# Performance work log

Hardware: AMD Instinct MI355X
Metric: run time of the kernel (lower is better)

The kernel has to match this reference:

```python
import jax, jax.numpy as jnp
import numpy as np

MODEL_SR = 50000
START_FRAME = int(MODEL_SR * 0.25)   # 12500
END_FRAME = int(MODEL_SR * 2.75)     # 137500
N_TAPS = 10000
BATCH = 64
T = 150000


def setup_inputs() -> dict:
    key = jax.random.key(0)
    k1, k2 = jax.random.split(key)
    x = jax.random.normal(k1, (BATCH, T), dtype=jnp.float32)          # mono audio clips
    ir = jax.random.normal(k2, (N_TAPS, 2), dtype=jnp.float32)        # BRIR: (taps, L/R)
    return {"x": x, "ir": ir}


def reference(x, ir):
    # Faithful to torch: ir flipped along taps, then cross-correlated by conv1d
    # (lax.conv_general_dilated is also cross-correlation), i.e. true convolution.
    n_taps = ir.shape[0]
    w = jnp.flip(ir, axis=0).T[:, None, :]              # (C_out=2, C_in=1, K)
    xp = jnp.pad(x, ((0, 0), (n_taps - 1, 0)))[:, None, :]  # left-pad K-1 -> (N, 1, T+K-1)
    y = jax.lax.conv_general_dilated(
        xp, w,
        window_strides=(1,),
        padding="VALID",
        dimension_numbers=("NCW", "OIW", "NCW"),
    )                                                    # (N, 2, T)
    return y[:, :, START_FRAME:END_FRAME]                # (N, 2, 125000)
```

## Files before the change

kernel.cpp:

```cpp
#include <hip/hip_runtime.h>


#define K_TAPS  10000
#define T_LEN   150000
#define OUT_T0  12500
#define OUT_T1  137500
#define OUT_LEN 125000
#define BATCH   64

#define TM    256
#define KC    32
#define NC    321
#define D0    10016
#define RROWS 288
#define ACOLS 40
#define XCOLS 40

typedef short  bf16x8 __attribute__((ext_vector_type(8)));
typedef float  f32x4  __attribute__((ext_vector_type(4)));

__device__ __forceinline__ unsigned f2bf(float f) {
    unsigned u = __builtin_bit_cast(unsigned, f);
    return (u + 0x7FFFu + ((u >> 16) & 1u)) >> 16;
}

__global__ __launch_bounds__(512, 4) void spatialize_mfma(
    const float* __restrict__ x, const float* __restrict__ ir,
    float* __restrict__ out)
{
    __shared__ ushort a_lds[2][RROWS][ACOLS];
    __shared__ ushort xb[2][BATCH][XCOLS];

    const int tid  = threadIdx.x;
    const int lane = tid & 63;
    const int wid  = tid >> 6;
    const int wm   = wid >> 1;
    const int wn   = wid & 1;
    const int t0   = OUT_T0 + blockIdx.x * TM;
    const int p_start = t0 - D0;

    const int bch = tid >> 8;
    const int bm  = (tid >> 3) & 31;
    const int bk0 = (tid & 7) * 4;

    const int sb = tid >> 3;
    const int sg = tid & 7;

#pragma unroll
    for (int s = 0; s < TM / KC; ++s) {
        const int m  = s * KC + bm;
        const int pr = KC + m;
        const int db = D0 + m - bk0;
        unsigned h0 = (db-0 >= 0 && db-0 < K_TAPS) ? f2bf(ir[2*(db-0)+bch]) : 0u;
        unsigned h1 = (db-1 >= 0 && db-1 < K_TAPS) ? f2bf(ir[2*(db-1)+bch]) : 0u;
        unsigned h2 = (db-2 >= 0 && db-2 < K_TAPS) ? f2bf(ir[2*(db-2)+bch]) : 0u;
        unsigned h3 = (db-3 >= 0 && db-3 < K_TAPS) ? f2bf(ir[2*(db-3)+bch]) : 0u;
        uint2 w; w.x = h0 | (h1 << 16); w.y = h2 | (h3 << 16);
        *reinterpret_cast<uint2*>(&a_lds[bch][pr][bk0]) = w;
    }
    {
        const float4 v = *reinterpret_cast<const float4*>(
            &x[(size_t)sb * T_LEN + p_start + sg * 4]);
        uint2 w; w.x = f2bf(v.x) | (f2bf(v.y) << 16);
                 w.y = f2bf(v.z) | (f2bf(v.w) << 16);
        *reinterpret_cast<uint2*>(&xb[0][sb][sg * 4]) = w;
    }
    __syncthreads();

    f32x4 acc[4][2][2];
#pragma unroll
    for (int mt = 0; mt < 4; ++mt)
#pragma unroll
        for (int nt = 0; nt < 2; ++nt)
#pragma unroll
            for (int ch = 0; ch < 2; ++ch)
                acc[mt][nt][ch] = (f32x4){0.f, 0.f, 0.f, 0.f};

    int vbase = KC;

    const int koff = 8 * (lane >> 4);
    const int lrow = lane & 15;

    for (int i = 0; i < NC; ++i) {
        const int  cur  = i & 1;
        const bool more = (i + 1 < NC);
        int vb2 = vbase - KC; if (vb2 < 0) vb2 += RROWS;

        float4 xv = make_float4(0.f, 0.f, 0.f, 0.f);
        float hv0 = 0.f, hv1 = 0.f, hv2 = 0.f, hv3 = 0.f;
        if (more) {
            const int p0n = p_start + (i + 1) * KC;
            xv = *reinterpret_cast<const float4*>(
                &x[(size_t)sb * T_LEN + p0n + sg * 4]);
            const int db = (D0 - (i + 1) * KC) + bm - bk0;
            hv0 = (db-0 >= 0 && db-0 < K_TAPS) ? ir[2*(db-0)+bch] : 0.f;
            hv1 = (db-1 >= 0 && db-1 < K_TAPS) ? ir[2*(db-1)+bch] : 0.f;
            hv2 = (db-2 >= 0 && db-2 < K_TAPS) ? ir[2*(db-2)+bch] : 0.f;
            hv3 = (db-3 >= 0 && db-3 < K_TAPS) ? ir[2*(db-3)+bch] : 0.f;
        }

        bf16x8 bfr0 = *reinterpret_cast<const bf16x8*>(&xb[cur][wn*32 +      lrow][koff]);
        bf16x8 bfr1 = *reinterpret_cast<const bf16x8*>(&xb[cur][wn*32 + 16 + lrow][koff]);
#pragma unroll
        for (int mt = 0; mt < 4; ++mt) {
            int g = vbase + wm * 64 + mt * 16; if (g >= RROWS) g -= RROWS;
            const int row = g + lrow;
#pragma unroll
            for (int ch = 0; ch < 2; ++ch) {
                bf16x8 af = *reinterpret_cast<const bf16x8*>(&a_lds[ch][row][koff]);
                acc[mt][0][ch] = __builtin_amdgcn_mfma_f32_16x16x32_bf16(
                    af, bfr0, acc[mt][0][ch], 0, 0, 0);
                acc[mt][1][ch] = __builtin_amdgcn_mfma_f32_16x16x32_bf16(
                    af, bfr1, acc[mt][1][ch], 0, 0, 0);
            }
        }

        if (more) {
            uint2 wx; wx.x = f2bf(xv.x) | (f2bf(xv.y) << 16);
                      wx.y = f2bf(xv.z) | (f2bf(xv.w) << 16);
            *reinterpret_cast<uint2*>(&xb[cur ^ 1][sb][sg * 4]) = wx;
            uint2 wa; wa.x = f2bf(hv0) | (f2bf(hv1) << 16);
                      wa.y = f2bf(hv2) | (f2bf(hv3) << 16);
            *reinterpret_cast<uint2*>(&a_lds[bch][vb2 + bm][bk0]) = wa;
            vbase = vb2;
        }
        __syncthreads();
    }

    const int r4 = (lane >> 4) * 4;
#pragma unroll
    for (int mt = 0; mt < 4; ++mt) {
        const int t4 = t0 + (wm * 4 + mt) * 16 + r4;
        if (t4 < OUT_T1) {
#pragma unroll
            for (int nt = 0; nt < 2; ++nt) {
                const int b = wn * 32 + nt * 16 + lrow;
#pragma unroll
                for (int ch = 0; ch < 2; ++ch) {
                    float4 v = make_float4(acc[mt][nt][ch][0], acc[mt][nt][ch][1],
                                           acc[mt][nt][ch][2], acc[mt][nt][ch][3]);
                    *reinterpret_cast<float4*>(
                        &out[(size_t)b * (2 * OUT_LEN) + (size_t)ch * OUT_LEN +
                             (t4 - OUT_T0)]) = v;
                }
            }
        }
    }
}

extern "C" void kernel_launch(void* const* d_in, const int* in_sizes, int n_in,
                              void* d_out, int out_size, void* d_ws, size_t ws_size,
                              hipStream_t stream)
{
    (void)in_sizes; (void)n_in; (void)d_ws; (void)ws_size; (void)out_size;
    const float* x  = (const float*)d_in[0];
    const float* ir = (const float*)d_in[1];
    float* out      = (float*)d_out;

    dim3 grid((OUT_LEN + TM - 1) / TM);
    dim3 block(512);
    hipLaunchKernelGGL(spatialize_mfma, grid, block, 0, stream, x, ir, out);
}
```

Before: 491.6 us.

## Precompute bf16 Toeplitz filter table in global memory and widen per-wave tiles

```diff
diff --git a/kernel.cpp b/kernel.cpp
--- a/kernel.cpp
+++ b/kernel.cpp
@@ -10,10 +10,14 @@
 
 #define TM    256
 #define KC    32
+#define D0    10016
 #define NC    321
-#define D0    10016
-#define RROWS 288
-#define ACOLS 40
+#define NMAX  (D0 + TM - 1)
+#define NTAB  10528
+#define CS_BYTES  (NTAB * 2)
+#define CH_STRIDE (8 * CS_BYTES)
+#define TAB_BYTES (2 * CH_STRIDE)
+
 #define XCOLS 40
 
 typedef short  bf16x8 __attribute__((ext_vector_type(8)));
@@ -24,124 +28,127 @@
     return (u + 0x7FFFu + ((u >> 16) & 1u)) >> 16;
 }
 
-__global__ __launch_bounds__(512, 4) void spatialize_mfma(
-    const float* __restrict__ x, const float* __restrict__ ir,
+__global__ __launch_bounds__(256) void build_tab(
+    const float* __restrict__ ir, ushort* __restrict__ tab)
+{
+    const int m = blockIdx.x * 256 + threadIdx.x;
+    if (m >= NTAB) return;
+    const int y   = blockIdx.y;
+    const int ch  = y >> 3;
+    const int rho = y & 7;
+    const int d   = NMAX - m - rho;
+    const float v = (d >= 0 && d < K_TAPS) ? ir[2 * d + ch] : 0.f;
+    tab[(size_t)ch * (8 * NTAB) + (size_t)rho * NTAB + m] = (ushort)f2bf(v);
+}
+
+__global__ __launch_bounds__(256, 2) void spatialize_mfma2(
+    const float* __restrict__ x, const ushort* __restrict__ tab,
     float* __restrict__ out)
 {
-    __shared__ ushort a_lds[2][RROWS][ACOLS];
     __shared__ ushort xb[2][BATCH][XCOLS];
 
     const int tid  = threadIdx.x;
     const int lane = tid & 63;
-    const int wid  = tid >> 6;
-    const int wm   = wid >> 1;
-    const int wn   = wid & 1;
-    const int t0   = OUT_T0 + blockIdx.x * TM;
+    const int wm   = tid >> 6;
+    const int lrow = lane & 15;
+    const int koff = (lane >> 4) * 8;
+
+    const int nwg = gridDim.x;
+    const int q8 = nwg >> 3, r8 = nwg & 7;
+    const int xcd = blockIdx.x & 7, loc = blockIdx.x >> 3;
+    const int tile = (xcd < r8 ? xcd * (q8 + 1) : r8 * (q8 + 1) + (xcd - r8) * q8) + loc;
+
+    const int t0      = OUT_T0 + tile * TM;
     const int p_start = t0 - D0;
 
-    const int bch = tid >> 8;
-    const int bm  = (tid >> 3) & 31;
-    const int bk0 = (tid & 7) * 4;
+    const int s0 = NMAX - D0 - wm * 64 - lrow + koff;
+    int aoff = (s0 & 7) * CS_BYTES + ((s0 >> 3) << 4);
+    const char* tA0 = (const char*)tab;
+    const char* tA1 = (const char*)tab + CH_STRIDE;
 
-    const int sb = tid >> 3;
-    const int sg = tid & 7;
+    const int sb = tid >> 2;
+    const int sg = tid & 3;
+    const float* xrow = x + (size_t)sb * T_LEN + p_start + sg * 8;
 
-#pragma unroll
-    for (int s = 0; s < TM / KC; ++s) {
-        const int m  = s * KC + bm;
-        const int pr = KC + m;
-        const int db = D0 + m - bk0;
-        unsigned h0 = (db-0 >= 0 && db-0 < K_TAPS) ? f2bf(ir[2*(db-0)+bch]) : 0u;
-        unsigned h1 = (db-1 >= 0 && db-1 < K_TAPS) ? f2bf(ir[2*(db-1)+bch]) : 0u;
-        unsigned h2 = (db-2 >= 0 && db-2 < K_TAPS) ? f2bf(ir[2*(db-2)+bch]) : 0u;
-        unsigned h3 = (db-3 >= 0 && db-3 < K_TAPS) ? f2bf(ir[2*(db-3)+bch]) : 0u;
-        uint2 w; w.x = h0 | (h1 << 16); w.y = h2 | (h3 << 16);
-        *reinterpret_cast<uint2*>(&a_lds[bch][pr][bk0]) = w;
-    }
     {
-        const float4 v = *reinterpret_cast<const float4*>(
-            &x[(size_t)sb * T_LEN + p_start + sg * 4]);
-        uint2 w; w.x = f2bf(v.x) | (f2bf(v.y) << 16);
-                 w.y = f2bf(v.z) | (f2bf(v.w) << 16);
-        *reinterpret_cast<uint2*>(&xb[0][sb][sg * 4]) = w;
+        const float4 v0 = *(const float4*)(xrow);
+        const float4 v1 = *(const float4*)(xrow + 4);
+        uint4 w;
+        w.x = f2bf(v0.x) | (f2bf(v0.y) << 16);
+        w.y = f2bf(v0.z) | (f2bf(v0.w) << 16);
+        w.z = f2bf(v1.x) | (f2bf(v1.y) << 16);
+        w.w = f2bf(v1.z) | (f2bf(v1.w) << 16);
+        *(uint4*)&xb[0][sb][sg * 8] = w;
     }
     __syncthreads();
 
-    f32x4 acc[4][2][2];
+    f32x4 acc[4][4][2];
 #pragma unroll
     for (int mt = 0; mt < 4; ++mt)
 #pragma unroll
-        for (int nt = 0; nt < 2; ++nt)
+        for (int nt = 0; nt < 4; ++nt)
 #pragma unroll
             for (int ch = 0; ch < 2; ++ch)
                 acc[mt][nt][ch] = (f32x4){0.f, 0.f, 0.f, 0.f};
 
-    int vbase = KC;
-
-    const int koff = 8 * (lane >> 4);
-    const int lrow = lane & 15;
-
     for (int i = 0; i < NC; ++i) {
         const int  cur  = i & 1;
         const bool more = (i + 1 < NC);
-        int vb2 = vbase - KC; if (vb2 < 0) vb2 += RROWS;
 
-        float4 xv = make_float4(0.f, 0.f, 0.f, 0.f);
-        float hv0 = 0.f, hv1 = 0.f, hv2 = 0.f, hv3 = 0.f;
+        float4 v0, v1;
         if (more) {
-            const int p0n = p_start + (i + 1) * KC;
-            xv = *reinterpret_cast<const float4*>(
-                &x[(size_t)sb * T_LEN + p0n + sg * 4]);
-            const int db = (D0 - (i + 1) * KC) + bm - bk0;
-            hv0 = (db-0 >= 0 && db-0 < K_TAPS) ? ir[2*(db-0)+bch] : 0.f;
-            hv1 = (db-1 >= 0 && db-1 < K_TAPS) ? ir[2*(db-1)+bch] : 0.f;
-            hv2 = (db-2 >= 0 && db-2 < K_TAPS) ? ir[2*(db-2)+bch] : 0.f;
-            hv3 = (db-3 >= 0 && db-3 < K_TAPS) ? ir[2*(db-3)+bch] : 0.f;
+            const float* xp = xrow + (i + 1) * KC;
+            v0 = *(const float4*)(xp);
+            v1 = *(const float4*)(xp + 4);
         }
 
-        bf16x8 bfr0 = *reinterpret_cast<const bf16x8*>(&xb[cur][wn*32 +      lrow][koff]);
-        bf16x8 bfr1 = *reinterpret_cast<const bf16x8*>(&xb[cur][wn*32 + 16 + lrow][koff]);
+        bf16x8 af0[4], af1[4];
 #pragma unroll
         for (int mt = 0; mt < 4; ++mt) {
-            int g = vbase + wm * 64 + mt * 16; if (g >= RROWS) g -= RROWS;
-            const int row = g + lrow;
+            af0[mt] = *(const bf16x8*)(tA0 + (aoff - 32 * mt));
+            af1[mt] = *(const bf16x8*)(tA1 + (aoff - 32 * mt));
+        }
+        bf16x8 bfr[4];
 #pragma unroll
-            for (int ch = 0; ch < 2; ++ch) {
-                bf16x8 af = *reinterpret_cast<const bf16x8*>(&a_lds[ch][row][koff]);
-                acc[mt][0][ch] = __builtin_amdgcn_mfma_f32_16x16x32_bf16(
-                    af, bfr0, acc[mt][0][ch], 0, 0, 0);
-                acc[mt][1][ch] = __builtin_amdgcn_mfma_f32_16x16x32_bf16(
-                    af, bfr1, acc[mt][1][ch], 0, 0, 0);
+        for (int nt = 0; nt < 4; ++nt)
+            bfr[nt] = *(const bf16x8*)&xb[cur][nt * 16 + lrow][koff];
+
+#pragma unroll
+        for (int mt = 0; mt < 4; ++mt)
+#pragma unroll
+            for (int nt = 0; nt < 4; ++nt) {
+                acc[mt][nt][0] = __builtin_amdgcn_mfma_f32_16x16x32_bf16(
+                    af0[mt], bfr[nt], acc[mt][nt][0], 0, 0, 0);
+                acc[mt][nt][1] = __builtin_amdgcn_mfma_f32_16x16x32_bf16(
+                    af1[mt], bfr[nt], acc[mt][nt][1], 0, 0, 0);
             }
-        }
 
         if (more) {
-            uint2 wx; wx.x = f2bf(xv.x) | (f2bf(xv.y) << 16);
-                      wx.y = f2bf(xv.z) | (f2bf(xv.w) << 16);
-            *reinterpret_cast<uint2*>(&xb[cur ^ 1][sb][sg * 4]) = wx;
-            uint2 wa; wa.x = f2bf(hv0) | (f2bf(hv1) << 16);
-                      wa.y = f2bf(hv2) | (f2bf(hv3) << 16);
-            *reinterpret_cast<uint2*>(&a_lds[bch][vb2 + bm][bk0]) = wa;
-            vbase = vb2;
+            uint4 w;
+            w.x = f2bf(v0.x) | (f2bf(v0.y) << 16);
+            w.y = f2bf(v0.z) | (f2bf(v0.w) << 16);
+            w.z = f2bf(v1.x) | (f2bf(v1.y) << 16);
+            w.w = f2bf(v1.z) | (f2bf(v1.w) << 16);
+            *(uint4*)&xb[cur ^ 1][sb][sg * 8] = w;
         }
         __syncthreads();
+        aoff += 64;
     }
 
     const int r4 = (lane >> 4) * 4;
 #pragma unroll
     for (int mt = 0; mt < 4; ++mt) {
-        const int t4 = t0 + (wm * 4 + mt) * 16 + r4;
+        const int t4 = t0 + wm * 64 + mt * 16 + r4;
         if (t4 < OUT_T1) {
 #pragma unroll
-            for (int nt = 0; nt < 2; ++nt) {
-                const int b = wn * 32 + nt * 16 + lrow;
+            for (int nt = 0; nt < 4; ++nt) {
+                const int b = nt * 16 + lrow;
 #pragma unroll
                 for (int ch = 0; ch < 2; ++ch) {
-                    float4 v = make_float4(acc[mt][nt][ch][0], acc[mt][nt][ch][1],
-                                           acc[mt][nt][ch][2], acc[mt][nt][ch][3]);
-                    *reinterpret_cast<float4*>(
-                        &out[(size_t)b * (2 * OUT_LEN) + (size_t)ch * OUT_LEN +
-                             (t4 - OUT_T0)]) = v;
+                    const f32x4 a = acc[mt][nt][ch];
+                    *(float4*)&out[(size_t)b * (2 * OUT_LEN) +
+                                   (size_t)ch * OUT_LEN + (t4 - OUT_T0)] =
+                        make_float4(a[0], a[1], a[2], a[3]);
                 }
             }
         }
@@ -152,12 +159,15 @@
                               void* d_out, int out_size, void* d_ws, size_t ws_size,
                               hipStream_t stream)
 {
-    (void)in_sizes; (void)n_in; (void)d_ws; (void)ws_size; (void)out_size;
+    (void)in_sizes; (void)n_in; (void)out_size; (void)ws_size;
     const float* x  = (const float*)d_in[0];
     const float* ir = (const float*)d_in[1];
     float* out      = (float*)d_out;
+    ushort* tab     = (ushort*)d_ws;
+
+    dim3 gt((NTAB + 255) / 256, 16);
+    hipLaunchKernelGGL(build_tab, gt, dim3(256), 0, stream, ir, tab);
 
     dim3 grid((OUT_LEN + TM - 1) / TM);
-    dim3 block(512);
-    hipLaunchKernelGGL(spatialize_mfma, grid, block, 0, stream, x, ir, out);
+    hipLaunchKernelGGL(spatialize_mfma2, grid, dim3(256), 0, stream, x, tab, out);
 }
```

Result: slower. 642.6 us (+30.7%).
